# Performance work log

Hardware: AMD Instinct MI355X
Metric: run time of the kernel (lower is better)

The kernel has to match this reference:

```python
import jax, jax.numpy as jnp
import numpy as np

HEADS = 4
OUT_CH = 32
IN_CH = 128
HC = HEADS * OUT_CH  # 128
N = 100000
G = 1000
E = 1600000
EG = 16000
NEG_SLOPE = 0.2


def gat_conv(x, edge_index, W, att_src, att_dst, bias):
    """PyG-style GATConv (concat heads, self-loops, leaky_relu 0.2, eval mode)."""
    n = x.shape[0]
    loop = jnp.arange(n)
    src = jnp.concatenate([edge_index[0], loop])
    dst = jnp.concatenate([edge_index[1], loop])
    h = (x @ W).reshape(n, HEADS, OUT_CH)            # [n,H,C]
    a_src = (h * att_src).sum(-1)                    # [n,H]
    a_dst = (h * att_dst).sum(-1)                    # [n,H]
    e = jax.nn.leaky_relu(a_src[src] + a_dst[dst], NEG_SLOPE)  # [e,H]
    m = jax.ops.segment_max(e, dst, num_segments=n)
    ex = jnp.exp(e - m[dst])
    s = jax.ops.segment_sum(ex, dst, num_segments=n)
    alpha = ex / (s[dst] + 1e-16)
    out = jax.ops.segment_sum(alpha[:, :, None] * h[src], dst, num_segments=n)
    return out.reshape(n, HC) + bias


def setup_inputs() -> dict:
    key = jax.random.key(0)
    ks = jax.random.split(key, 16)
    inv = 1.0 / np.sqrt(IN_CH)
    invh = 1.0 / np.sqrt(HC)
    return {
        "x": jax.random.normal(ks[0], (N, IN_CH), jnp.float32),
        "x_g": jax.random.normal(ks[1], (G, IN_CH), jnp.float32),
        "edge_index": jax.random.randint(ks[2], (2, E), 0, N, jnp.int32),
        "edge_index_g": jax.random.randint(ks[3], (2, EG), 0, G, jnp.int32),
        "node_group": jax.random.randint(ks[4], (N,), 0, G, jnp.int32),
        "W1": jax.random.normal(ks[5], (IN_CH, HC), jnp.float32) * inv,
        "att_src1": jax.random.normal(ks[6], (HEADS, OUT_CH), jnp.float32) * invh,
        "att_dst1": jax.random.normal(ks[7], (HEADS, OUT_CH), jnp.float32) * invh,
        "bias1": jnp.zeros((HC,), jnp.float32),
        "W2": jax.random.normal(ks[8], (IN_CH, HC), jnp.float32) * inv,
        "att_src2": jax.random.normal(ks[9], (HEADS, OUT_CH), jnp.float32) * invh,
        "att_dst2": jax.random.normal(ks[10], (HEADS, OUT_CH), jnp.float32) * invh,
        "bias2": jnp.zeros((HC,), jnp.float32),
        "W_fc": jax.random.normal(ks[11], (HC, OUT_CH), jnp.float32) * invh,
        "b_fc": jnp.zeros((OUT_CH,), jnp.float32),
    }


def reference(x, x_g, edge_index, edge_index_g, node_group,
              W1, att_src1, att_dst1, bias1,
              W2, att_src2, att_dst2, bias2, W_fc, b_fc):
    x_out = gat_conv(x, edge_index, W1, att_src1, att_dst1, bias1)      # [N,HC]
    x_g_out = gat_conv(x_g, edge_index_g, W2, att_src2, att_dst2, bias2)  # [G,HC]

    # mean of adjacent group features per group (segment mean over group edges)
    adj_sum = jax.ops.segment_sum(x_g_out[edge_index_g[1]], edge_index_g[0], num_segments=G)
    cnt = jax.ops.segment_sum(jnp.ones((edge_index_g.shape[1],), x_g_out.dtype),
                              edge_index_g[0], num_segments=G)
    adj_mean = adj_sum / jnp.maximum(cnt, 1.0)[:, None]                  # [G,HC]

    gf = x_g_out[node_group]          # per-node own-group feature   [N,HC]
    af = adj_mean[node_group]         # per-node adjacent-group mean [N,HC]
    imp_g = jnp.einsum('nc,nc->n', x_out, gf)
    imp_a = jnp.einsum('nc,nc->n', x_out, af)
    upd = x_out + imp_g[:, None] * gf + imp_a[:, None] * af
    out = upd @ W_fc + b_fc
    return out, x_g_out
```

## Files before the change

kernel.cpp:

```cpp
#include <hip/hip_runtime.h>

__host__ __device__ static inline int imin(int a, int b) { return a < b ? a : b; }

__device__ __forceinline__ float lrelu(float v) { return v > 0.f ? v : 0.2f * v; }

__device__ __forceinline__ void online_upd(float& m, float& s, float e) {
  float M = fmaxf(m, e);
  s = s * __expf(m - M) + __expf(e - M);
  m = M;
}
__device__ __forceinline__ void online_merge(float& m, float& s, float mo, float so) {
  float M = fmaxf(m, mo);
  s = s * __expf(m - M) + so * __expf(mo - M);
  m = M;
}

__global__ __launch_bounds__(256) void gemm128(const float* __restrict__ X,
                                               const float* __restrict__ W,
                                               float* __restrict__ H, int n) {
  __shared__ float Wl[128 * 128];
  __shared__ float Xl[4][4 * 128];
  const int tid = threadIdx.x;
  for (int i = tid; i < 4096; i += 256)
    ((float4*)Wl)[i] = ((const float4*)W)[i];
  __syncthreads();

  const int wave = tid >> 6, lane = tid & 63;
  const int nb = (n + 15) >> 4;
  for (int tb = blockIdx.x; tb < nb; tb += gridDim.x) {
    const int rbase = tb * 16 + wave * 4;
    float2* xl2 = (float2*)&Xl[wave][0];
#pragma unroll
    for (int rr = 0; rr < 4; ++rr) {
      int r = rbase + rr;
      float2 v = make_float2(0.f, 0.f);
      if (r < n) v = ((const float2*)(X + (size_t)r * 128))[lane];
      xl2[rr * 64 + lane] = v;
    }
    float a0[4] = {0, 0, 0, 0}, a1[4] = {0, 0, 0, 0};
#pragma unroll 4
    for (int c = 0; c < 128; ++c) {
      float w0 = Wl[c * 128 + lane];
      float w1 = Wl[c * 128 + lane + 64];
#pragma unroll
      for (int rr = 0; rr < 4; ++rr) {
        float xc = Xl[wave][rr * 128 + c];
        a0[rr] = fmaf(xc, w0, a0[rr]);
        a1[rr] = fmaf(xc, w1, a1[rr]);
      }
    }
#pragma unroll
    for (int rr = 0; rr < 4; ++rr) {
      int r = rbase + rr;
      if (r < n) {
        H[(size_t)r * 128 + lane] = a0[rr];
        H[(size_t)r * 128 + lane + 64] = a1[rr];
      }
    }
  }
}

__global__ __launch_bounds__(256) void att_scores(const float* __restrict__ H,
                                                  const float* __restrict__ att_s,
                                                  const float* __restrict__ att_d,
                                                  float* __restrict__ asrc,
                                                  float* __restrict__ adst, int n) {
  long long idx = (long long)blockIdx.x * 256 + threadIdx.x;
  if (idx >= (long long)n * 128) return;
  int c = (int)(idx & 127);
  float h = H[idx];
  float ps = h * att_s[c];
  float pd = h * att_d[c];
#pragma unroll
  for (int m = 16; m >= 1; m >>= 1) {
    ps += __shfl_xor(ps, m);
    pd += __shfl_xor(pd, m);
  }
  if ((c & 31) == 0) {
    long long node = idx >> 7;
    int head = c >> 5;
    asrc[node * 4 + head] = ps;
    adst[node * 4 + head] = pd;
  }
}

__global__ __launch_bounds__(256) void count_deg(const int* __restrict__ dst, int ne,
                                                 int* __restrict__ deg) {
  int i = blockIdx.x * 256 + threadIdx.x;
  if (i < ne) atomicAdd(&deg[dst[i]], 1);
}

__global__ __launch_bounds__(256) void scan_part1(const int* __restrict__ in, int n,
                                                  int* __restrict__ bsum) {
  int base = blockIdx.x * 4096 + threadIdx.x * 16;
  int s = 0;
  if (base + 16 <= n) {
    const int4* p = (const int4*)(in + base);
#pragma unroll
    for (int k = 0; k < 4; ++k) {
      int4 v = p[k];
      s += v.x + v.y + v.z + v.w;
    }
  } else {
    for (int k = 0; k < 16; ++k) {
      int i = base + k;
      if (i < n) s += in[i];
    }
  }
#pragma unroll
  for (int o = 1; o < 64; o <<= 1) s += __shfl_xor(s, o);
  __shared__ int ws[4];
  int wave = threadIdx.x >> 6, lane = threadIdx.x & 63;
  if (lane == 0) ws[wave] = s;
  __syncthreads();
  if (threadIdx.x == 0) bsum[blockIdx.x] = ws[0] + ws[1] + ws[2] + ws[3];
}

__global__ __launch_bounds__(256) void scan_part2(int* __restrict__ bsum, int nb,
                                                  int* __restrict__ off, int n) {
  __shared__ int sm[256];
  int tid = threadIdx.x;
  int v = (tid < nb) ? bsum[tid] : 0;
  sm[tid] = v;
  __syncthreads();
  int x = v;
  for (int o = 1; o < 256; o <<= 1) {
    int t = (tid >= o) ? sm[tid - o] : 0;
    __syncthreads();
    x += t;
    sm[tid] = x;
    __syncthreads();
  }
  if (tid < nb) bsum[tid] = x - v;
  if (tid == 0) off[n] = sm[255];
}

__global__ __launch_bounds__(256) void scan_part3(const int* __restrict__ in, int n,
                                                  const int* __restrict__ bsum,
                                                  int* __restrict__ out) {
  int tid = threadIdx.x;
  int base = blockIdx.x * 4096 + tid * 16;
  int vals[16];
  if (base + 16 <= n) {
    const int4* p = (const int4*)(in + base);
#pragma unroll
    for (int k = 0; k < 4; ++k) {
      int4 v = p[k];
      vals[4 * k] = v.x;
      vals[4 * k + 1] = v.y;
      vals[4 * k + 2] = v.z;
      vals[4 * k + 3] = v.w;
    }
  } else {
#pragma unroll
    for (int k = 0; k < 16; ++k) {
      int i = base + k;
      vals[k] = (i < n) ? in[i] : 0;
    }
  }
  int tsum = 0;
#pragma unroll
  for (int k = 0; k < 16; ++k) tsum += vals[k];
  int lane = tid & 63, wave = tid >> 6;
  int inc = tsum;
#pragma unroll
  for (int o = 1; o < 64; o <<= 1) {
    int t = __shfl_up(inc, o);
    if (lane >= o) inc += t;
  }
  int exc = inc - tsum;
  __shared__ int ws[4];
  if (lane == 63) ws[wave] = inc;
  __syncthreads();
  int woff = 0;
  for (int w = 0; w < wave; ++w) woff += ws[w];
  int off0 = bsum[blockIdx.x] + woff + exc;
  int run = 0;
#pragma unroll
  for (int k = 0; k < 16; ++k) {
    int i = base + k;
    if (i < n) out[i] = off0 + run;
    run += vals[k];
  }
}

__global__ __launch_bounds__(256) void fill_csr(const int* __restrict__ src,
                                                const int* __restrict__ dst, int ne,
                                                const int* __restrict__ off,
                                                int* __restrict__ cur,
                                                int* __restrict__ csr) {
  int i = blockIdx.x * 256 + threadIdx.x;
  if (i < ne) {
    int d = dst[i];
    int p = atomicAdd(&cur[d], 1);
    csr[off[d] + p] = src[i];
  }
}

__global__ __launch_bounds__(256) void gat_aggregate(
    const float* __restrict__ H, const float* __restrict__ asrc,
    const float* __restrict__ adst, const int* __restrict__ off,
    const int* __restrict__ csr, const float* __restrict__ bias,
    float* __restrict__ out, int n) {
  int gw = (blockIdx.x * 256 + threadIdx.x) >> 6;
  if (gw >= n) return;
  int lane = threadIdx.x & 63;
  int n0 = off[gw];
  int deg = off[gw + 1] - n0;

  float4 ad = ((const float4*)adst)[gw];
  float m0 = -1e30f, m1 = -1e30f, m2 = -1e30f, m3 = -1e30f;
  float s0 = 0.f, s1 = 0.f, s2 = 0.f, s3 = 0.f;

  for (int i = lane; i < deg; i += 64) {
    int sr = csr[n0 + i];
    float4 as = ((const float4*)asrc)[sr];
    online_upd(m0, s0, lrelu(as.x + ad.x));
    online_upd(m1, s1, lrelu(as.y + ad.y));
    online_upd(m2, s2, lrelu(as.z + ad.z));
    online_upd(m3, s3, lrelu(as.w + ad.w));
  }
#pragma unroll
  for (int o = 1; o < 64; o <<= 1) {
    online_merge(m0, s0, __shfl_xor(m0, o), __shfl_xor(s0, o));
    online_merge(m1, s1, __shfl_xor(m1, o), __shfl_xor(s1, o));
    online_merge(m2, s2, __shfl_xor(m2, o), __shfl_xor(s2, o));
    online_merge(m3, s3, __shfl_xor(m3, o), __shfl_xor(s3, o));
  }
  float4 asn = ((const float4*)asrc)[gw];
  float e0 = lrelu(asn.x + ad.x), e1 = lrelu(asn.y + ad.y);
  float e2 = lrelu(asn.z + ad.z), e3 = lrelu(asn.w + ad.w);
  online_upd(m0, s0, e0);
  online_upd(m1, s1, e1);
  online_upd(m2, s2, e2);
  online_upd(m3, s3, e3);

  int c0 = lane * 2;
  int hd = lane >> 4;
  float m_h = (hd == 0) ? m0 : (hd == 1) ? m1 : (hd == 2) ? m2 : m3;
  float s_h = (hd == 0) ? s0 : (hd == 1) ? s1 : (hd == 2) ? s2 : s3;
  float ad_h = (hd == 0) ? ad.x : (hd == 1) ? ad.y : (hd == 2) ? ad.z : ad.w;
  float es_h = (hd == 0) ? e0 : (hd == 1) ? e1 : (hd == 2) ? e2 : e3;
  float inv = 1.f / (s_h + 1e-16f);

  const float* hn = H + (size_t)gw * 128;
  float aself = __expf(es_h - m_h) * inv;
  float acc0 = aself * hn[c0];
  float acc1 = aself * hn[c0 + 1];

  for (int base = 0; base < deg; base += 64) {
    int cnt = imin(64, deg - base);
    int sreg = (base + lane < deg) ? csr[n0 + base + lane] : 0;
    for (int j = 0; j < cnt; ++j) {
      int sr = __shfl(sreg, j);
      float av = asrc[(size_t)sr * 4 + hd];
      float al = __expf(lrelu(av + ad_h) - m_h) * inv;
      float2 hv = ((const float2*)(H + (size_t)sr * 128))[lane];
      acc0 = fmaf(al, hv.x, acc0);
      acc1 = fmaf(al, hv.y, acc1);
    }
  }
  out[(size_t)gw * 128 + c0] = acc0 + bias[c0];
  out[(size_t)gw * 128 + c0 + 1] = acc1 + bias[c0 + 1];
}

__global__ __launch_bounds__(256) void adj_accum(const int* __restrict__ gsrc,
                                                 const int* __restrict__ gdst,
                                                 const float* __restrict__ xgout,
                                                 float* __restrict__ adj,
                                                 float* __restrict__ cnt, int ne) {
  int idx = blockIdx.x * 256 + threadIdx.x;
  if (idx >= ne * 64) return;
  int e = idx >> 6;
  int l = idx & 63;
  int gs = gsrc[e], gd = gdst[e];
  float2 v = ((const float2*)(xgout + (size_t)gd * 128))[l];
  atomicAdd(&adj[(size_t)gs * 128 + 2 * l], v.x);
  atomicAdd(&adj[(size_t)gs * 128 + 2 * l + 1], v.y);
  if (l == 0) atomicAdd(&cnt[gs], 1.0f);
}

__global__ __launch_bounds__(256) void adj_mean_k(float* __restrict__ adj,
                                                  const float* __restrict__ cnt,
                                                  int total) {
  int i = blockIdx.x * 256 + threadIdx.x;
  if (i < total) adj[i] /= fmaxf(cnt[i >> 7], 1.0f);
}

__global__ __launch_bounds__(256) void final_fuse(
    const float* __restrict__ xout, const float* __restrict__ xgout,
    const float* __restrict__ adjm, const int* __restrict__ ngrp,
    const float* __restrict__ Wfc, const float* __restrict__ bfc,
    float* __restrict__ out, int n) {
  __shared__ float Wl[128 * 32];
  __shared__ float up[4][128];
  int tid = threadIdx.x;
  for (int i = tid; i < 1024; i += 256)
    ((float4*)Wl)[i] = ((const float4*)Wfc)[i];
  __syncthreads();

  int wave = tid >> 6, lane = tid & 63;
  int tw = gridDim.x * 4;
  for (int node = blockIdx.x * 4 + wave; node < n; node += tw) {
    int g = ngrp[node];
    float2 xo = ((const float2*)(xout + (size_t)node * 128))[lane];
    float2 gf = ((const float2*)(xgout + (size_t)g * 128))[lane];
    float2 af = ((const float2*)(adjm + (size_t)g * 128))[lane];
    float pg = xo.x * gf.x + xo.y * gf.y;
    float pa = xo.x * af.x + xo.y * af.y;
#pragma unroll
    for (int o = 1; o < 64; o <<= 1) {
      pg += __shfl_xor(pg, o);
      pa += __shfl_xor(pa, o);
    }
    float u0 = xo.x + pg * gf.x + pa * af.x;
    float u1 = xo.y + pg * gf.y + pa * af.y;
    up[wave][lane * 2] = u0;
    up[wave][lane * 2 + 1] = u1;
    int j = lane & 31;
    int ch = (lane >> 5) * 64;
    float acc = 0.f;
#pragma unroll 8
    for (int cc = 0; cc < 64; ++cc)
      acc = fmaf(up[wave][ch + cc], Wl[(ch + cc) * 32 + j], acc);
    acc += __shfl_xor(acc, 32);
    if (lane < 32) out[(size_t)node * 32 + j] = acc + bfc[j];
  }
}

extern "C" void kernel_launch(void* const* d_in, const int* in_sizes, int n_in,
                              void* d_out, int out_size, void* d_ws, size_t ws_size,
                              hipStream_t stream) {
  const float* x = (const float*)d_in[0];
  const float* xg = (const float*)d_in[1];
  const int* ei = (const int*)d_in[2];
  const int* eig = (const int*)d_in[3];
  const int* ngrp = (const int*)d_in[4];
  const float* W1 = (const float*)d_in[5];
  const float* as1 = (const float*)d_in[6];
  const float* ad1 = (const float*)d_in[7];
  const float* b1 = (const float*)d_in[8];
  const float* W2 = (const float*)d_in[9];
  const float* as2 = (const float*)d_in[10];
  const float* ad2 = (const float*)d_in[11];
  const float* b2 = (const float*)d_in[12];
  const float* Wfc = (const float*)d_in[13];
  const float* bfc = (const float*)d_in[14];

  const int N = in_sizes[0] / 128;
  const int G = in_sizes[1] / 128;
  const int E = in_sizes[2] / 2;
  const int EG = in_sizes[3] / 2;

  char* p = (char*)d_ws;
  auto carve = [&](size_t bytes) {
    void* r = (void*)p;
    p += (bytes + 255) & ~(size_t)255;
    return r;
  };
  float* h1 = (float*)carve((size_t)N * 128 * 4);
  float* xout = (float*)carve((size_t)N * 128 * 4);
  float* asrc1 = (float*)carve((size_t)N * 16);
  float* adst1 = (float*)carve((size_t)N * 16);
  int* off1 = (int*)carve((size_t)(N + 1) * 4);
  int* deg1 = (int*)carve((size_t)N * 4);
  int* csr1 = (int*)carve((size_t)E * 4);
  float* h2 = (float*)carve((size_t)G * 128 * 4);
  float* asrc2 = (float*)carve((size_t)G * 16);
  float* adst2 = (float*)carve((size_t)G * 16);
  int* off2 = (int*)carve((size_t)(G + 1) * 4);
  int* deg2 = (int*)carve((size_t)G * 4);
  int* csr2 = (int*)carve((size_t)EG * 4);
  float* adjm = (float*)carve((size_t)G * 128 * 4);
  float* cnt = (float*)carve((size_t)G * 4);
  int* bsum1 = (int*)carve(256 * 4);
  int* bsum2 = (int*)carve(256 * 4);

  float* outN = (float*)d_out;
  float* xgout = (float*)d_out + (size_t)N * 32;

  const int* src1 = ei;
  const int* dst1 = ei + E;
  const int* srcg = eig;
  const int* dstg = eig + EG;

  hipMemsetAsync(deg1, 0, (size_t)N * 4, stream);
  hipMemsetAsync(deg2, 0, (size_t)G * 4, stream);
  hipMemsetAsync(adjm, 0, (size_t)G * 128 * 4, stream);
  hipMemsetAsync(cnt, 0, (size_t)G * 4, stream);

  gemm128<<<imin((N + 15) / 16, 2048), 256, 0, stream>>>(x, W1, h1, N);
  gemm128<<<imin((G + 15) / 16, 2048), 256, 0, stream>>>(xg, W2, h2, G);
  att_scores<<<(int)(((long long)N * 128 + 255) / 256), 256, 0, stream>>>(h1, as1, ad1, asrc1, adst1, N);
  att_scores<<<(int)(((long long)G * 128 + 255) / 256), 256, 0, stream>>>(h2, as2, ad2, asrc2, adst2, G);
  count_deg<<<(E + 255) / 256, 256, 0, stream>>>(dst1, E, deg1);
  count_deg<<<(EG + 255) / 256, 256, 0, stream>>>(dstg, EG, deg2);

  const int nb1 = (N + 4095) / 4096;
  const int nb2 = (G + 4095) / 4096;
  scan_part1<<<nb1, 256, 0, stream>>>(deg1, N, bsum1);
  scan_part2<<<1, 256, 0, stream>>>(bsum1, nb1, off1, N);
  scan_part3<<<nb1, 256, 0, stream>>>(deg1, N, bsum1, off1);
  scan_part1<<<nb2, 256, 0, stream>>>(deg2, G, bsum2);
  scan_part2<<<1, 256, 0, stream>>>(bsum2, nb2, off2, G);
  scan_part3<<<nb2, 256, 0, stream>>>(deg2, G, bsum2, off2);

  hipMemsetAsync(deg1, 0, (size_t)N * 4, stream);
  hipMemsetAsync(deg2, 0, (size_t)G * 4, stream);
  fill_csr<<<(E + 255) / 256, 256, 0, stream>>>(src1, dst1, E, off1, deg1, csr1);
  fill_csr<<<(EG + 255) / 256, 256, 0, stream>>>(srcg, dstg, EG, off2, deg2, csr2);
  gat_aggregate<<<(N + 3) / 4, 256, 0, stream>>>(h1, asrc1, adst1, off1, csr1, b1, xout, N);
  gat_aggregate<<<(G + 3) / 4, 256, 0, stream>>>(h2, asrc2, adst2, off2, csr2, b2, xgout, G);
  adj_accum<<<(EG * 64 + 255) / 256, 256, 0, stream>>>(srcg, dstg, xgout, adjm, cnt, EG);
  adj_mean_k<<<(G * 128 + 255) / 256, 256, 0, stream>>>(adjm, cnt, G * 128);
  final_fuse<<<2048, 256, 0, stream>>>(xout, xgout, adjm, ngrp, Wfc, bfc, outN, N);
}
```

Baseline: 680.5 us.

## Fuse attention scores into GEMM and use single-pass softmax aggregation

The attention-score dot products are now computed inside the GEMM epilogue with wave shuffles, which removes the separate att_scores kernel and its reread of H. The GAT aggregation drops the online max/sum pass and computes the exponentials once per edge, stages them in shared memory and accumulates unnormalized weighted features, dividing by the sum at the end. This halves the per-edge passes over the CSR and asrc gathers. In exchange, skipping max subtraction risks overflow if scores grow large, and the shared-memory exchange relies on wave-synchronous behaviour with no barrier.

```diff
diff --git a/kernel.cpp b/kernel.cpp
--- a/kernel.cpp
+++ b/kernel.cpp
@@ -3,21 +3,14 @@
 __host__ __device__ static inline int imin(int a, int b) { return a < b ? a : b; }
 
 __device__ __forceinline__ float lrelu(float v) { return v > 0.f ? v : 0.2f * v; }
-
-__device__ __forceinline__ void online_upd(float& m, float& s, float e) {
-  float M = fmaxf(m, e);
-  s = s * __expf(m - M) + __expf(e - M);
-  m = M;
-}
-__device__ __forceinline__ void online_merge(float& m, float& s, float mo, float so) {
-  float M = fmaxf(m, mo);
-  s = s * __expf(m - M) + so * __expf(mo - M);
-  m = M;
-}
 
 __global__ __launch_bounds__(256) void gemm128(const float* __restrict__ X,
                                                const float* __restrict__ W,
-                                               float* __restrict__ H, int n) {
+                                               const float* __restrict__ att_s,
+                                               const float* __restrict__ att_d,
+                                               float* __restrict__ H,
+                                               float* __restrict__ asrc,
+                                               float* __restrict__ adst, int n) {
   __shared__ float Wl[128 * 128];
   __shared__ float Xl[4][4 * 128];
   const int tid = threadIdx.x;
@@ -26,6 +19,8 @@
   __syncthreads();
 
   const int wave = tid >> 6, lane = tid & 63;
+  const float as_l = att_s[lane], as_h = att_s[lane + 64];
+  const float ad_l = att_d[lane], ad_h = att_d[lane + 64];
   const int nb = (n + 15) >> 4;
   for (int tb = blockIdx.x; tb < nb; tb += gridDim.x) {
     const int rbase = tb * 16 + wave * 4;
@@ -55,32 +50,28 @@
       if (r < n) {
         H[(size_t)r * 128 + lane] = a0[rr];
         H[(size_t)r * 128 + lane + 64] = a1[rr];
+        float ps0 = a0[rr] * as_l, pd0 = a0[rr] * ad_l;
+        float ps1 = a1[rr] * as_h, pd1 = a1[rr] * ad_h;
+#pragma unroll
+        for (int m = 16; m >= 1; m >>= 1) {
+          ps0 += __shfl_xor(ps0, m);
+          pd0 += __shfl_xor(pd0, m);
+          ps1 += __shfl_xor(ps1, m);
+          pd1 += __shfl_xor(pd1, m);
+        }
+        if (lane == 0) {
+          asrc[(size_t)r * 4 + 0] = ps0;
+          adst[(size_t)r * 4 + 0] = pd0;
+          asrc[(size_t)r * 4 + 2] = ps1;
+          adst[(size_t)r * 4 + 2] = pd1;
+        } else if (lane == 32) {
+          asrc[(size_t)r * 4 + 1] = ps0;
+          adst[(size_t)r * 4 + 1] = pd0;
+          asrc[(size_t)r * 4 + 3] = ps1;
+          adst[(size_t)r * 4 + 3] = pd1;
+        }
       }
     }
-  }
-}
-
-__global__ __launch_bounds__(256) void att_scores(const float* __restrict__ H,
-                                                  const float* __restrict__ att_s,
-                                                  const float* __restrict__ att_d,
-                                                  float* __restrict__ asrc,
-                                                  float* __restrict__ adst, int n) {
-  long long idx = (long long)blockIdx.x * 256 + threadIdx.x;
-  if (idx >= (long long)n * 128) return;
-  int c = (int)(idx & 127);
-  float h = H[idx];
-  float ps = h * att_s[c];
-  float pd = h * att_d[c];
-#pragma unroll
-  for (int m = 16; m >= 1; m >>= 1) {
-    ps += __shfl_xor(ps, m);
-    pd += __shfl_xor(pd, m);
-  }
-  if ((c & 31) == 0) {
-    long long node = idx >> 7;
-    int head = c >> 5;
-    asrc[node * 4 + head] = ps;
-    adst[node * 4 + head] = pd;
   }
 }
 
@@ -202,66 +193,71 @@
     const float* __restrict__ adst, const int* __restrict__ off,
     const int* __restrict__ csr, const float* __restrict__ bias,
     float* __restrict__ out, int n) {
+  __shared__ float4 exl[4][64];
   int gw = (blockIdx.x * 256 + threadIdx.x) >> 6;
   if (gw >= n) return;
-  int lane = threadIdx.x & 63;
+  int wave = (threadIdx.x >> 6), lane = threadIdx.x & 63;
   int n0 = off[gw];
   int deg = off[gw + 1] - n0;
 
   float4 ad = ((const float4*)adst)[gw];
-  float m0 = -1e30f, m1 = -1e30f, m2 = -1e30f, m3 = -1e30f;
-  float s0 = 0.f, s1 = 0.f, s2 = 0.f, s3 = 0.f;
-
-  for (int i = lane; i < deg; i += 64) {
-    int sr = csr[n0 + i];
-    float4 as = ((const float4*)asrc)[sr];
-    online_upd(m0, s0, lrelu(as.x + ad.x));
-    online_upd(m1, s1, lrelu(as.y + ad.y));
-    online_upd(m2, s2, lrelu(as.z + ad.z));
-    online_upd(m3, s3, lrelu(as.w + ad.w));
-  }
-#pragma unroll
-  for (int o = 1; o < 64; o <<= 1) {
-    online_merge(m0, s0, __shfl_xor(m0, o), __shfl_xor(s0, o));
-    online_merge(m1, s1, __shfl_xor(m1, o), __shfl_xor(s1, o));
-    online_merge(m2, s2, __shfl_xor(m2, o), __shfl_xor(s2, o));
-    online_merge(m3, s3, __shfl_xor(m3, o), __shfl_xor(s3, o));
-  }
-  float4 asn = ((const float4*)asrc)[gw];
-  float e0 = lrelu(asn.x + ad.x), e1 = lrelu(asn.y + ad.y);
-  float e2 = lrelu(asn.z + ad.z), e3 = lrelu(asn.w + ad.w);
-  online_upd(m0, s0, e0);
-  online_upd(m1, s1, e1);
-  online_upd(m2, s2, e2);
-  online_upd(m3, s3, e3);
-
   int c0 = lane * 2;
   int hd = lane >> 4;
-  float m_h = (hd == 0) ? m0 : (hd == 1) ? m1 : (hd == 2) ? m2 : m3;
-  float s_h = (hd == 0) ? s0 : (hd == 1) ? s1 : (hd == 2) ? s2 : s3;
-  float ad_h = (hd == 0) ? ad.x : (hd == 1) ? ad.y : (hd == 2) ? ad.z : ad.w;
-  float es_h = (hd == 0) ? e0 : (hd == 1) ? e1 : (hd == 2) ? e2 : e3;
+  float4 s4 = make_float4(0.f, 0.f, 0.f, 0.f);
+  float acc0 = 0.f, acc1 = 0.f;
+  const float* exw = (const float*)&exl[wave][0];
+
+  for (int base = 0; base < deg; base += 64) {
+    int idx = base + lane;
+    bool v = idx < deg;
+    int sr = v ? csr[n0 + idx] : 0;
+    float4 ex = make_float4(0.f, 0.f, 0.f, 0.f);
+    if (v) {
+      float4 as = ((const float4*)asrc)[sr];
+      ex.x = __expf(lrelu(as.x + ad.x));
+      ex.y = __expf(lrelu(as.y + ad.y));
+      ex.z = __expf(lrelu(as.z + ad.z));
+      ex.w = __expf(lrelu(as.w + ad.w));
+      s4.x += ex.x;
+      s4.y += ex.y;
+      s4.z += ex.z;
+      s4.w += ex.w;
+    }
+    exl[wave][lane] = ex;
+    int cnt = imin(64, deg - base);
+    for (int j = 0; j < cnt; ++j) {
+      int srj = __shfl(sr, j);
+      float exh = exw[j * 4 + hd];
+      float2 hv = ((const float2*)(H + (size_t)srj * 128))[lane];
+      acc0 = fmaf(exh, hv.x, acc0);
+      acc1 = fmaf(exh, hv.y, acc1);
+    }
+  }
+#pragma unroll
+  for (int o = 1; o < 64; o <<= 1) {
+    s4.x += __shfl_xor(s4.x, o);
+    s4.y += __shfl_xor(s4.y, o);
+    s4.z += __shfl_xor(s4.z, o);
+    s4.w += __shfl_xor(s4.w, o);
+  }
+  float4 asn = ((const float4*)asrc)[gw];
+  float4 exs;
+  exs.x = __expf(lrelu(asn.x + ad.x));
+  exs.y = __expf(lrelu(asn.y + ad.y));
+  exs.z = __expf(lrelu(asn.z + ad.z));
+  exs.w = __expf(lrelu(asn.w + ad.w));
+  s4.x += exs.x;
+  s4.y += exs.y;
+  s4.z += exs.z;
+  s4.w += exs.w;
+  float s_h = (hd == 0) ? s4.x : (hd == 1) ? s4.y : (hd == 2) ? s4.z : s4.w;
+  float e_h = (hd == 0) ? exs.x : (hd == 1) ? exs.y : (hd == 2) ? exs.z : exs.w;
+  float2 hs = ((const float2*)(H + (size_t)gw * 128))[lane];
+  acc0 = fmaf(e_h, hs.x, acc0);
+  acc1 = fmaf(e_h, hs.y, acc1);
   float inv = 1.f / (s_h + 1e-16f);
-
-  const float* hn = H + (size_t)gw * 128;
-  float aself = __expf(es_h - m_h) * inv;
-  float acc0 = aself * hn[c0];
-  float acc1 = aself * hn[c0 + 1];
-
-  for (int base = 0; base < deg; base += 64) {
-    int cnt = imin(64, deg - base);
-    int sreg = (base + lane < deg) ? csr[n0 + base + lane] : 0;
-    for (int j = 0; j < cnt; ++j) {
-      int sr = __shfl(sreg, j);
-      float av = asrc[(size_t)sr * 4 + hd];
-      float al = __expf(lrelu(av + ad_h) - m_h) * inv;
-      float2 hv = ((const float2*)(H + (size_t)sr * 128))[lane];
-      acc0 = fmaf(al, hv.x, acc0);
-      acc1 = fmaf(al, hv.y, acc1);
-    }
-  }
-  out[(size_t)gw * 128 + c0] = acc0 + bias[c0];
-  out[(size_t)gw * 128 + c0 + 1] = acc1 + bias[c0 + 1];
+  out[(size_t)gw * 128 + c0] = acc0 * inv + bias[c0];
+  out[(size_t)gw * 128 + c0 + 1] = acc1 * inv + bias[c0 + 1];
 }
 
 __global__ __launch_bounds__(256) void adj_accum(const int* __restrict__ gsrc,
@@ -389,10 +385,8 @@
   hipMemsetAsync(adjm, 0, (size_t)G * 128 * 4, stream);
   hipMemsetAsync(cnt, 0, (size_t)G * 4, stream);
 
-  gemm128<<<imin((N + 15) / 16, 2048), 256, 0, stream>>>(x, W1, h1, N);
-  gemm128<<<imin((G + 15) / 16, 2048), 256, 0, stream>>>(xg, W2, h2, G);
-  att_scores<<<(int)(((long long)N * 128 + 255) / 256), 256, 0, stream>>>(h1, as1, ad1, asrc1, adst1, N);
-  att_scores<<<(int)(((long long)G * 128 + 255) / 256), 256, 0, stream>>>(h2, as2, ad2, asrc2, adst2, G);
+  gemm128<<<imin((N + 15) / 16, 2048), 256, 0, stream>>>(x, W1, as1, ad1, h1, asrc1, adst1, N);
+  gemm128<<<imin((G + 15) / 16, 2048), 256, 0, stream>>>(xg, W2, as2, ad2, h2, asrc2, adst2, G);
   count_deg<<<(E + 255) / 256, 256, 0, stream>>>(dst1, E, deg1);
   count_deg<<<(EG + 255) / 256, 256, 0, stream>>>(dstg, EG, deg2);
 
```

Measured after the change: 660.4 us. -3.0%, faster.
